# Performance work log

Measured on AMD Instinct MI355X. Metric: run time of the kernel, lower is better.

## Reference

```python
import jax, jax.numpy as jnp
import numpy as np

R = 32            # voxel resolution
DIM = 240         # channels C
EPS_NORM = 0.0    # module eps
BN_EPS = 1e-5     # torch BatchNorm1d default eps


def setup_inputs() -> dict:
    key = jax.random.key(0)
    k1, k2, k3 = jax.random.split(key, 3)
    B, C, N = 4, DIM, 32768
    features = jax.random.normal(k1, (B, C, N), jnp.float32)
    coords = jax.random.uniform(k2, (B, 3, N), jnp.float32)
    # mlp params: Conv1d(2C -> C, kernel 1) + BatchNorm1d(C)
    w = jax.random.normal(k3, (C, 2 * C), jnp.float32) / np.sqrt(2 * C).astype(np.float32)
    b = jnp.zeros((C,), jnp.float32)
    gamma = jnp.ones((C,), jnp.float32)
    beta = jnp.zeros((C,), jnp.float32)
    return {"features": features, "coords": coords, "w": w, "b": b, "gamma": gamma, "beta": beta}


def _voxelize(features, coords):
    # normalize coords into [0, 1], scale to voxel grid
    nc = coords - coords.mean(axis=2, keepdims=True)                      # [B,3,N]
    scale = jnp.linalg.norm(nc, axis=1, keepdims=True).max(axis=2, keepdims=True) * 2.0 + EPS_NORM
    nc = nc / scale + 0.5
    nc = jnp.clip(nc * R, 0, R - 1)
    vox = jnp.round(nc).astype(jnp.int32)
    pos = vox[:, 0] + vox[:, 1] * R + vox[:, 2] * (R * R)                 # [B,N] flattened voxel id
    R3 = R * R * R

    def per_batch(f, p):
        # f: [C,N], p: [N] -> [2C, R3]; per-voxel max feature + second (min) feature
        mx = jax.ops.segment_max(f.T, p, num_segments=R3)                 # [R3, C]
        mn = jax.ops.segment_min(f.T, p, num_segments=R3)                 # [R3, C]
        cnt = jax.ops.segment_sum(jnp.ones_like(p), p, num_segments=R3)  # [R3]
        mask = (cnt > 0)[:, None]
        mx = jnp.where(mask, mx, 0.0)
        mn = jnp.where(mask, mn, 0.0)
        return jnp.concatenate([mx, mn], axis=1).T                        # [2C, R3]

    fea = jax.vmap(per_batch)(features, pos)                              # [B,2C,R3]
    return fea, nc


def reference(features, coords, w, b, gamma, beta):
    fea, nc = _voxelize(features, coords)
    # 1x1 Conv1d (pointwise GEMM) + BatchNorm1d (training-mode batch stats) + Swish
    y = jnp.einsum('co,bov->bcv', w, fea) + b[None, :, None]
    mean = y.mean(axis=(0, 2), keepdims=True)
    var = y.var(axis=(0, 2), keepdims=True)
    y = gamma[None, :, None] * (y - mean) * jax.lax.rsqrt(var + BN_EPS) + beta[None, :, None]
    y = y * jax.nn.sigmoid(y)
    B, C, _ = features.shape
    return y.reshape(B, C, R, R, R), nc
```

## Files before the change

kernel.cpp:

```cpp
#include <hip/hip_runtime.h>
#include <cstdint>
#include <cstddef>

#define RR 32
#define R3 32768
#define NPT 32768
#define CH 240
#define CH2 480
#define NB 4
#define Y_ELEMS 31457280

typedef __attribute__((ext_vector_type(8))) short short8v;
typedef __attribute__((ext_vector_type(4))) float float4v;

union u8pack { short8v v; unsigned short u[8]; };

static __device__ __forceinline__ float bf2f(unsigned short u) {
  return __uint_as_float(((unsigned int)u) << 16);
}
static __device__ __forceinline__ unsigned short f2bf(float f) {
  unsigned int u = __float_as_uint(f);
  u = (u + 0x7FFFu + ((u >> 16) & 1u)) >> 16;
  return (unsigned short)u;
}

static __device__ __forceinline__ void gl_lds16(const void* g, void* l) {
  __builtin_amdgcn_global_load_lds((const __attribute__((address_space(1))) unsigned int*)g,
                                   (__attribute__((address_space(3))) unsigned int*)l, 16, 0, 0);
}

__global__ void k_init(int* __restrict__ cnt, float* __restrict__ stats,
                       const float* __restrict__ w, unsigned short* __restrict__ wfrag) {
  int g = blockIdx.x * 256 + threadIdx.x;
  if (g < NB * R3) cnt[g] = 0;
  if (g < 1024) stats[g] = 0.0f;
  if (g < 14400) {
    int kc = g / 960, rem = g % 960;
    int m = rem >> 6, l = rem & 63;
    int ln = l & 15, q = l >> 4;
    const float* src = w + (size_t)(m * 16 + ln) * CH2 + kc * 32 + q * 8;
    u8pack pk;
#pragma unroll
    for (int j = 0; j < 8; j++) pk.u[j] = f2bf(src[j]);
    *(short8v*)&wfrag[(size_t)g * 8] = pk.v;
  }
}

__global__ __launch_bounds__(1024) void k_coord_stats(const float* __restrict__ coords,
                                                      float* __restrict__ ms) {
  __shared__ float red[1024];
  __shared__ float mean[3];
  int b = blockIdx.x, t = threadIdx.x;
  const float4* cb4 = (const float4*)(coords + (size_t)b * 3 * NPT);
  float s[3] = {0.f, 0.f, 0.f};
  for (int i = t; i < NPT / 4; i += 1024) {
#pragma unroll
    for (int d = 0; d < 3; d++) {
      float4 v = cb4[d * (NPT / 4) + i];
      s[d] += (v.x + v.y) + (v.z + v.w);
    }
  }
  for (int d = 0; d < 3; d++) {
    red[t] = s[d]; __syncthreads();
    for (int k = 512; k > 0; k >>= 1) { if (t < k) red[t] += red[t + k]; __syncthreads(); }
    if (t == 0) mean[d] = red[0] * (1.0f / NPT);
    __syncthreads();
  }
  float m0 = mean[0], m1 = mean[1], m2 = mean[2];
  float mx = 0.f;
  for (int i = t; i < NPT / 4; i += 1024) {
    float4 x = cb4[i], y = cb4[NPT / 4 + i], z = cb4[2 * (NPT / 4) + i];
    float dx, dy, dz, n;
    dx = x.x - m0; dy = y.x - m1; dz = z.x - m2; n = dx * dx + dy * dy + dz * dz; mx = fmaxf(mx, n);
    dx = x.y - m0; dy = y.y - m1; dz = z.y - m2; n = dx * dx + dy * dy + dz * dz; mx = fmaxf(mx, n);
    dx = x.z - m0; dy = y.z - m1; dz = z.z - m2; n = dx * dx + dy * dy + dz * dz; mx = fmaxf(mx, n);
    dx = x.w - m0; dy = y.w - m1; dz = z.w - m2; n = dx * dx + dy * dy + dz * dz; mx = fmaxf(mx, n);
  }
  red[t] = mx; __syncthreads();
  for (int k = 512; k > 0; k >>= 1) { if (t < k) red[t] = fmaxf(red[t], red[t + k]); __syncthreads(); }
  if (t == 0) {
    ms[b * 4 + 0] = m0; ms[b * 4 + 1] = m1; ms[b * 4 + 2] = m2;
    ms[b * 4 + 3] = sqrtf(red[0]) * 2.0f;
  }
}

__global__ void k_pos_nc(const float* __restrict__ coords, const float* __restrict__ ms,
                         float* __restrict__ ncout, int* __restrict__ pos, int* __restrict__ cnt) {
  int g = blockIdx.x * 256 + threadIdx.x;
  int b = g >> 15, i = g & (NPT - 1);
  const float* cb = coords + (size_t)b * 3 * NPT;
  float scale = ms[b * 4 + 3];
  int vox[3];
#pragma unroll
  for (int d = 0; d < 3; d++) {
    float v = (cb[(size_t)d * NPT + i] - ms[b * 4 + d]) / scale + 0.5f;
    v = fminf(fmaxf(v * (float)RR, 0.0f), (float)(RR - 1));
    ncout[((size_t)(b * 3 + d)) * NPT + i] = v;
    vox[d] = (int)rintf(v);
  }
  int p = (b << 15) | (vox[0] + (vox[1] << 5) + (vox[2] << 10));
  pos[g] = p;
  atomicAdd(&cnt[p], 1);
}

__global__ void k_scan(const int* __restrict__ cnt, int* __restrict__ offs) {
  __shared__ int part[1024];
  int b = blockIdx.x, t = threadIdx.x;
  const int base = b * R3;
  int local[32];
  int s = 0;
#pragma unroll
  for (int j = 0; j < 32; j++) { local[j] = cnt[base + t * 32 + j]; s += local[j]; }
  part[t] = s; __syncthreads();
  for (int d = 1; d < 1024; d <<= 1) {
    int v = (t >= d) ? part[t - d] : 0;
    __syncthreads();
    part[t] += v;
    __syncthreads();
  }
  int run = (t == 0) ? 0 : part[t - 1];
#pragma unroll
  for (int j = 0; j < 32; j++) { offs[base + t * 32 + j] = run; run += local[j]; }
}

__global__ void k_scatter(const int* __restrict__ pos, int* __restrict__ offs,
                          int* __restrict__ sorted) {
  int g = blockIdx.x * 256 + threadIdx.x;
  int p = pos[g];
  int slot = atomicAdd(&offs[p], 1);
  sorted[((g >> 15) << 15) + slot] = g;
}

__global__ void k_transpose3(const float* __restrict__ f, unsigned short* __restrict__ ft) {
  __shared__ float tile[CH * 65];
  int p0 = blockIdx.x * 64, b = blockIdx.y;
  int t = threadIdx.x;
  {
    int pp = t & 63, cq = t >> 6;
    const float* src = f + ((size_t)b * CH) * NPT + p0 + pp;
#pragma unroll 4
    for (int j = 0; j < 60; ++j) {
      int c = j * 4 + cq;
      tile[c * 65 + pp] = src[(size_t)c * NPT];
    }
  }
  __syncthreads();
  int ch8 = t & 7;
#pragma unroll
  for (int pass = 0; pass < 2; ++pass) {
    int p = pass * 32 + (t >> 3);
    unsigned short* dst = ft + ((size_t)(b * NPT + p0 + p)) * CH;
#pragma unroll
    for (int i = 0; i < 4; ++i) {
      int ch = ch8 + 8 * i;
      if (ch < 30) {
        u8pack pk;
#pragma unroll
        for (int jj = 0; jj < 8; ++jj) pk.u[jj] = f2bf(tile[(ch * 8 + jj) * 65 + p]);
        *(short8v*)&dst[ch * 8] = pk.v;
      }
    }
  }
}

__global__ __launch_bounds__(256) void k_voxel4(const int* __restrict__ cnt,
                                                const int* __restrict__ offs,
                                                const int* __restrict__ sorted,
                                                const unsigned short* __restrict__ ft,
                                                unsigned short* __restrict__ feaf) {
  __shared__ unsigned short sh[7680];
  int bcg = blockIdx.x;
  int b = bcg >> 11;
  int wave = threadIdx.x >> 6, lane = threadIdx.x & 63;
  int sub = lane >> 5, l = lane & 31;
  int vbase = bcg << 4;
#pragma unroll
  for (int it = 0; it < 2; ++it) {
    int ln = wave + 8 * it + 4 * sub;
    if (l < 30) {
      int v = vbase + ln;
      int t0 = l, t1 = 30 + l;
      int idx0 = (t0 >> 2) * 512 + ((t0 & 3) * 16 + ln) * 8;
      int idx1 = (t1 >> 2) * 512 + ((t1 & 3) * 16 + ln) * 8;
      int n = cnt[v];
      if (n == 0) {
        u8pack z;
#pragma unroll
        for (int j = 0; j < 8; j++) z.u[j] = 0;
        *(short8v*)&sh[idx0] = z.v;
        *(short8v*)&sh[idx1] = z.v;
      } else {
        int start = offs[v] - n;
        const int* sp = sorted + (b << 15) + start;
        float mx[8], mn[8];
#pragma unroll
        for (int j = 0; j < 8; j++) { mx[j] = -__builtin_inff(); mn[j] = __builtin_inff(); }
        int j = 0;
        for (; j + 2 <= n; j += 2) {
          int r0 = sp[j], r1 = sp[j + 1];
          u8pack u0, u1;
          u0.v = *(const short8v*)(ft + (size_t)r0 * CH + l * 8);
          u1.v = *(const short8v*)(ft + (size_t)r1 * CH + l * 8);
#pragma unroll
          for (int k = 0; k < 8; k++) {
            float a = bf2f(u0.u[k]), c = bf2f(u1.u[k]);
            mx[k] = fmaxf(mx[k], fmaxf(a, c));
            mn[k] = fminf(mn[k], fminf(a, c));
          }
        }
        if (j < n) {
          int r0 = sp[j];
          u8pack u0;
          u0.v = *(const short8v*)(ft + (size_t)r0 * CH + l * 8);
#pragma unroll
          for (int k = 0; k < 8; k++) {
            float a = bf2f(u0.u[k]);
            mx[k] = fmaxf(mx[k], a);
            mn[k] = fminf(mn[k], a);
          }
        }
        u8pack omx, omn;
#pragma unroll
        for (int k = 0; k < 8; k++) { omx.u[k] = f2bf(mx[k]); omn.u[k] = f2bf(mn[k]); }
        *(short8v*)&sh[idx0] = omx.v;
        *(short8v*)&sh[idx1] = omn.v;
      }
    }
  }
  __syncthreads();
  unsigned short* dst = feaf + (size_t)bcg * 7680;
  for (int i = threadIdx.x; i < 960; i += 256)
    *(int4*)&dst[i * 8] = *(const int4*)&sh[i * 8];
}

__global__ __launch_bounds__(256, 2) void k_gemm5(const unsigned short* __restrict__ wfrag,
                                                  const unsigned short* __restrict__ feaf,
                                                  const float* __restrict__ bias,
                                                  float* __restrict__ out,
                                                  float* __restrict__ gstats) {
  __shared__ unsigned short wl0[7680];
  __shared__ unsigned short wl1[7680];
  __shared__ float bstats[2 * CH];
  for (int i = threadIdx.x; i < 2 * CH; i += 256) bstats[i] = 0.0f;

  int bz = blockIdx.z;
  int wave = threadIdx.x >> 6, lane = threadIdx.x & 63;
  int ln = lane & 15, q = lane >> 4;
  int v0 = blockIdx.x * 128 + wave * 32;
  int cg0 = v0 >> 4;

  float4v acc[15][2];
#pragma unroll
  for (int m = 0; m < 15; m++) {
    acc[m][0] = (float4v){0.f, 0.f, 0.f, 0.f};
    acc[m][1] = (float4v){0.f, 0.f, 0.f, 0.f};
  }

  const unsigned short* fb = feaf + ((size_t)(bz * 2048 + cg0) * 15) * 512 + lane * 8;

  short8v bc0, bc1, bn0, bn1;
  {
    const unsigned short* gs = wfrag + lane * 8;
    for (int i = wave; i < 15; i += 4) gl_lds16(gs + i * 512, wl0 + i * 512);
    bc0 = *(const short8v*)(fb);
    bc1 = *(const short8v*)(fb + (size_t)15 * 512);
  }

#pragma unroll
  for (int kc = 0; kc < 15; ++kc) {
    __syncthreads();
    if (kc < 14) {
      unsigned short* dstb = ((kc + 1) & 1) ? wl1 : wl0;
      const unsigned short* gs = wfrag + (size_t)(kc + 1) * 7680 + lane * 8;
      for (int i = wave; i < 15; i += 4) gl_lds16(gs + i * 512, dstb + i * 512);
      bn0 = *(const short8v*)(fb + (size_t)(kc + 1) * 512);
      bn1 = *(const short8v*)(fb + (size_t)(15 + kc + 1) * 512);
    }
    const unsigned short* wb = (kc & 1) ? wl1 : wl0;
    const unsigned short* wp = wb + lane * 8;
#pragma unroll
    for (int m = 0; m < 15; ++m) {
      short8v a = *(const short8v*)(wp + m * 512);
      acc[m][0] = __builtin_amdgcn_mfma_f32_16x16x32_bf16(a, bc0, acc[m][0], 0, 0, 0);
      acc[m][1] = __builtin_amdgcn_mfma_f32_16x16x32_bf16(a, bc1, acc[m][1], 0, 0, 0);
    }
    bc0 = bn0; bc1 = bn1;
  }

  float* o0 = out + (size_t)bz * CH * R3 + v0 + ln;
  float* o1 = o0 + 16;
#pragma unroll
  for (int m = 0; m < 15; ++m) {
    int cbase = m * 16 + q * 4;
    float s[4], sq[4];
#pragma unroll
    for (int r = 0; r < 4; ++r) {
      float bb = bias[cbase + r];
      float y0 = acc[m][0][r] + bb;
      float y1 = acc[m][1][r] + bb;
      o0[(size_t)(cbase + r) * R3] = y0;
      o1[(size_t)(cbase + r) * R3] = y1;
      s[r] = y0 + y1;
      sq[r] = y0 * y0 + y1 * y1;
    }
#pragma unroll
    for (int off = 1; off < 16; off <<= 1) {
#pragma unroll
      for (int r = 0; r < 4; ++r) {
        s[r] += __shfl_xor(s[r], off);
        sq[r] += __shfl_xor(sq[r], off);
      }
    }
    if (ln == 0) {
#pragma unroll
      for (int r = 0; r < 4; ++r) {
        atomicAdd(&bstats[cbase + r], s[r]);
        atomicAdd(&bstats[CH + cbase + r], sq[r]);
      }
    }
  }
  __syncthreads();
  for (int i = threadIdx.x; i < 2 * CH; i += 256) atomicAdd(&gstats[i], bstats[i]);
}

__global__ void k_apply(float* __restrict__ y, const float* __restrict__ stats,
                        const float* __restrict__ gamma, const float* __restrict__ beta) {
  int g = blockIdx.x * 256 + threadIdx.x;
  int c = (g >> 13) % CH;
  const float ninv = 1.0f / (float)(NB * R3);
  float mean = stats[c] * ninv;
  float var = stats[CH + c] * ninv - mean * mean;
  float s = gamma[c] * rsqrtf(var + 1e-5f);
  float h = beta[c] - mean * s;
  float4 v = ((const float4*)y)[g];
  float t0 = v.x * s + h; v.x = t0 / (1.0f + __expf(-t0));
  float t1 = v.y * s + h; v.y = t1 / (1.0f + __expf(-t1));
  float t2 = v.z * s + h; v.z = t2 / (1.0f + __expf(-t2));
  float t3 = v.w * s + h; v.w = t3 / (1.0f + __expf(-t3));
  ((float4*)y)[g] = v;
}

extern "C" void kernel_launch(void* const* d_in, const int* in_sizes, int n_in,
                              void* d_out, int out_size, void* d_ws, size_t ws_size,
                              hipStream_t stream) {
  const float* features = (const float*)d_in[0];
  const float* coords   = (const float*)d_in[1];
  const float* w        = (const float*)d_in[2];
  const float* bias     = (const float*)d_in[3];
  const float* gamma    = (const float*)d_in[4];
  const float* beta     = (const float*)d_in[5];
  float* out = (float*)d_out;

  char* ws = (char*)d_ws;
  size_t off = 0;
  float* ms    = (float*)(ws + off); off += 256;
  float* stats = (float*)(ws + off); off += 4096;
  int* pos     = (int*)(ws + off);   off += (size_t)NB * NPT * 4;
  int* cnt     = (int*)(ws + off);   off += (size_t)NB * R3 * 4;
  int* offs    = (int*)(ws + off);   off += (size_t)NB * R3 * 4;
  int* sorted  = (int*)(ws + off);   off += (size_t)NB * NPT * 4;
  unsigned short* wfrag = (unsigned short*)(ws + off); off += (size_t)CH * CH2 * 2;
  unsigned short* ft    = (unsigned short*)(ws + off); off += (size_t)NB * NPT * CH * 2;
  unsigned short* feaf  = (unsigned short*)(ws + off); off += (size_t)NB * R3 * CH2 * 2;

  float* ncout = out + Y_ELEMS;

  k_init<<<516, 256, 0, stream>>>(cnt, stats, w, wfrag);
  k_coord_stats<<<4, 1024, 0, stream>>>(coords, ms);
  k_pos_nc<<<512, 256, 0, stream>>>(coords, ms, ncout, pos, cnt);
  k_scan<<<4, 1024, 0, stream>>>(cnt, offs);
  k_scatter<<<512, 256, 0, stream>>>(pos, offs, sorted);
  k_transpose3<<<dim3(512, 4), 256, 0, stream>>>(features, ft);
  k_voxel4<<<NB * 2048, 256, 0, stream>>>(cnt, offs, sorted, ft, feaf);
  k_gemm5<<<dim3(256, 1, NB), 256, 0, stream>>>(wfrag, feaf, bias, out, stats);
  k_apply<<<Y_ELEMS / 1024, 256, 0, stream>>>(out, stats, gamma, beta);
}
```

Before: 421.7 us.

## Store pre-BN GEMM output as bf16 and retile GEMM with resident weight slice

The GEMM now writes its pre-normalization output as bf16 into a reused workspace buffer instead of fp32 into the final output, and the apply kernel reads bf16 and writes fp32. This halves the intermediate write and read traffic between GEMM and the BN/Swish pass. The GEMM is retiled so each block keeps an 80-channel slice of the weights fully resident in LDS and computes 64 voxels per wave, with the weight fragments reordered to match. That removes the per-k LDS double-buffer syncs, at the cost of reading the features once per channel group and adding bf16 rounding error to the output.

```diff
diff --git a/kernel.cpp b/kernel.cpp
--- a/kernel.cpp
+++ b/kernel.cpp
@@ -35,9 +35,11 @@
   if (g < NB * R3) cnt[g] = 0;
   if (g < 1024) stats[g] = 0.0f;
   if (g < 14400) {
-    int kc = g / 960, rem = g % 960;
-    int m = rem >> 6, l = rem & 63;
-    int ln = l & 15, q = l >> 4;
+    int lane = g & 63, t = g >> 6;
+    int mg = t / 75, r = t % 75;
+    int kc = r / 5, mL = r % 5;
+    int m = mg * 5 + mL;
+    int ln = lane & 15, q = lane >> 4;
     const float* src = w + (size_t)(m * 16 + ln) * CH2 + kc * 32 + q * 8;
     u8pack pk;
 #pragma unroll
@@ -233,111 +235,120 @@
     *(int4*)&dst[i * 8] = *(const int4*)&sh[i * 8];
 }
 
-__global__ __launch_bounds__(256, 2) void k_gemm5(const unsigned short* __restrict__ wfrag,
+__global__ __launch_bounds__(256, 2) void k_gemm6(const unsigned short* __restrict__ wfrag,
                                                   const unsigned short* __restrict__ feaf,
                                                   const float* __restrict__ bias,
-                                                  float* __restrict__ out,
+                                                  unsigned short* __restrict__ ybf,
                                                   float* __restrict__ gstats) {
-  __shared__ unsigned short wl0[7680];
-  __shared__ unsigned short wl1[7680];
-  __shared__ float bstats[2 * CH];
-  for (int i = threadIdx.x; i < 2 * CH; i += 256) bstats[i] = 0.0f;
-
-  int bz = blockIdx.z;
+  __shared__ unsigned short wl[75 * 512];
+  __shared__ float bstats[160];
   int wave = threadIdx.x >> 6, lane = threadIdx.x & 63;
   int ln = lane & 15, q = lane >> 4;
-  int v0 = blockIdx.x * 128 + wave * 32;
+  int mg = blockIdx.y, bz = blockIdx.z;
+
+  for (int i = threadIdx.x; i < 160; i += 256) bstats[i] = 0.0f;
+
+  {
+    const unsigned short* gs = wfrag + (size_t)mg * 75 * 512 + lane * 8;
+    for (int i = wave; i < 75; i += 4) gl_lds16(gs + i * 512, wl + i * 512);
+  }
+
+  int v0 = blockIdx.x * 256 + wave * 64;
   int cg0 = v0 >> 4;
-
-  float4v acc[15][2];
-#pragma unroll
-  for (int m = 0; m < 15; m++) {
-    acc[m][0] = (float4v){0.f, 0.f, 0.f, 0.f};
-    acc[m][1] = (float4v){0.f, 0.f, 0.f, 0.f};
-  }
-
-  const unsigned short* fb = feaf + ((size_t)(bz * 2048 + cg0) * 15) * 512 + lane * 8;
-
-  short8v bc0, bc1, bn0, bn1;
-  {
-    const unsigned short* gs = wfrag + lane * 8;
-    for (int i = wave; i < 15; i += 4) gl_lds16(gs + i * 512, wl0 + i * 512);
-    bc0 = *(const short8v*)(fb);
-    bc1 = *(const short8v*)(fb + (size_t)15 * 512);
-  }
+  const unsigned short* fbb = feaf + ((size_t)(bz * 2048 + cg0) * 15) * 512 + lane * 8;
+
+  float4v acc[5][4];
+#pragma unroll
+  for (int m = 0; m < 5; m++)
+#pragma unroll
+    for (int j = 0; j < 4; j++) acc[m][j] = (float4v){0.f, 0.f, 0.f, 0.f};
+
+  short8v cb0 = *(const short8v*)(fbb + (size_t)(0 * 15 + 0) * 512);
+  short8v cb1 = *(const short8v*)(fbb + (size_t)(1 * 15 + 0) * 512);
+  short8v cb2 = *(const short8v*)(fbb + (size_t)(2 * 15 + 0) * 512);
+  short8v cb3 = *(const short8v*)(fbb + (size_t)(3 * 15 + 0) * 512);
+
+  __syncthreads();
 
 #pragma unroll
   for (int kc = 0; kc < 15; ++kc) {
-    __syncthreads();
+    short8v nb0, nb1, nb2, nb3;
     if (kc < 14) {
-      unsigned short* dstb = ((kc + 1) & 1) ? wl1 : wl0;
-      const unsigned short* gs = wfrag + (size_t)(kc + 1) * 7680 + lane * 8;
-      for (int i = wave; i < 15; i += 4) gl_lds16(gs + i * 512, dstb + i * 512);
-      bn0 = *(const short8v*)(fb + (size_t)(kc + 1) * 512);
-      bn1 = *(const short8v*)(fb + (size_t)(15 + kc + 1) * 512);
-    }
-    const unsigned short* wb = (kc & 1) ? wl1 : wl0;
-    const unsigned short* wp = wb + lane * 8;
-#pragma unroll
-    for (int m = 0; m < 15; ++m) {
-      short8v a = *(const short8v*)(wp + m * 512);
-      acc[m][0] = __builtin_amdgcn_mfma_f32_16x16x32_bf16(a, bc0, acc[m][0], 0, 0, 0);
-      acc[m][1] = __builtin_amdgcn_mfma_f32_16x16x32_bf16(a, bc1, acc[m][1], 0, 0, 0);
-    }
-    bc0 = bn0; bc1 = bn1;
-  }
-
-  float* o0 = out + (size_t)bz * CH * R3 + v0 + ln;
-  float* o1 = o0 + 16;
-#pragma unroll
-  for (int m = 0; m < 15; ++m) {
-    int cbase = m * 16 + q * 4;
-    float s[4], sq[4];
+      nb0 = *(const short8v*)(fbb + (size_t)(0 * 15 + kc + 1) * 512);
+      nb1 = *(const short8v*)(fbb + (size_t)(1 * 15 + kc + 1) * 512);
+      nb2 = *(const short8v*)(fbb + (size_t)(2 * 15 + kc + 1) * 512);
+      nb3 = *(const short8v*)(fbb + (size_t)(3 * 15 + kc + 1) * 512);
+    }
+    const unsigned short* wp = wl + (size_t)(kc * 5) * 512 + lane * 8;
+#pragma unroll
+    for (int mL = 0; mL < 5; ++mL) {
+      short8v a = *(const short8v*)(wp + (size_t)mL * 512);
+      acc[mL][0] = __builtin_amdgcn_mfma_f32_16x16x32_bf16(a, cb0, acc[mL][0], 0, 0, 0);
+      acc[mL][1] = __builtin_amdgcn_mfma_f32_16x16x32_bf16(a, cb1, acc[mL][1], 0, 0, 0);
+      acc[mL][2] = __builtin_amdgcn_mfma_f32_16x16x32_bf16(a, cb2, acc[mL][2], 0, 0, 0);
+      acc[mL][3] = __builtin_amdgcn_mfma_f32_16x16x32_bf16(a, cb3, acc[mL][3], 0, 0, 0);
+    }
+    if (kc < 14) { cb0 = nb0; cb1 = nb1; cb2 = nb2; cb3 = nb3; }
+  }
+
+  unsigned short* yb = ybf + ((size_t)bz * CH) * R3 + v0 + ln;
+#pragma unroll
+  for (int mL = 0; mL < 5; ++mL) {
 #pragma unroll
     for (int r = 0; r < 4; ++r) {
-      float bb = bias[cbase + r];
-      float y0 = acc[m][0][r] + bb;
-      float y1 = acc[m][1][r] + bb;
-      o0[(size_t)(cbase + r) * R3] = y0;
-      o1[(size_t)(cbase + r) * R3] = y1;
-      s[r] = y0 + y1;
-      sq[r] = y0 * y0 + y1 * y1;
-    }
-#pragma unroll
-    for (int off = 1; off < 16; off <<= 1) {
-#pragma unroll
-      for (int r = 0; r < 4; ++r) {
-        s[r] += __shfl_xor(s[r], off);
-        sq[r] += __shfl_xor(sq[r], off);
+      int cl = mL * 16 + q * 4 + r;
+      int c = mg * 80 + cl;
+      float bb = bias[c];
+      float y0 = acc[mL][0][r] + bb;
+      float y1 = acc[mL][1][r] + bb;
+      float y2 = acc[mL][2][r] + bb;
+      float y3 = acc[mL][3][r] + bb;
+      unsigned short* yrow = yb + (size_t)c * R3;
+      yrow[0] = f2bf(y0); yrow[16] = f2bf(y1); yrow[32] = f2bf(y2); yrow[48] = f2bf(y3);
+      float s = (y0 + y1) + (y2 + y3);
+      float sq = (y0 * y0 + y1 * y1) + (y2 * y2 + y3 * y3);
+#pragma unroll
+      for (int off = 1; off < 16; off <<= 1) {
+        s += __shfl_xor(s, off);
+        sq += __shfl_xor(sq, off);
       }
-    }
-    if (ln == 0) {
-#pragma unroll
-      for (int r = 0; r < 4; ++r) {
-        atomicAdd(&bstats[cbase + r], s[r]);
-        atomicAdd(&bstats[CH + cbase + r], sq[r]);
+      if (ln == 0) {
+        atomicAdd(&bstats[cl], s);
+        atomicAdd(&bstats[80 + cl], sq);
       }
     }
   }
   __syncthreads();
-  for (int i = threadIdx.x; i < 2 * CH; i += 256) atomicAdd(&gstats[i], bstats[i]);
-}
-
-__global__ void k_apply(float* __restrict__ y, const float* __restrict__ stats,
-                        const float* __restrict__ gamma, const float* __restrict__ beta) {
+  for (int i = threadIdx.x; i < 160; i += 256) {
+    int g = (i < 80) ? (mg * 80 + i) : (CH + mg * 80 + (i - 80));
+    atomicAdd(&gstats[g], bstats[i]);
+  }
+}
+
+__global__ void k_apply(const unsigned short* __restrict__ ybf, float* __restrict__ out,
+                        const float* __restrict__ stats, const float* __restrict__ gamma,
+                        const float* __restrict__ beta) {
   int g = blockIdx.x * 256 + threadIdx.x;
-  int c = (g >> 13) % CH;
+  int c = (g >> 12) % CH;
   const float ninv = 1.0f / (float)(NB * R3);
   float mean = stats[c] * ninv;
   float var = stats[CH + c] * ninv - mean * mean;
   float s = gamma[c] * rsqrtf(var + 1e-5f);
   float h = beta[c] - mean * s;
-  float4 v = ((const float4*)y)[g];
-  float t0 = v.x * s + h; v.x = t0 / (1.0f + __expf(-t0));
-  float t1 = v.y * s + h; v.y = t1 / (1.0f + __expf(-t1));
-  float t2 = v.z * s + h; v.z = t2 / (1.0f + __expf(-t2));
-  float t3 = v.w * s + h; v.w = t3 / (1.0f + __expf(-t3));
-  ((float4*)y)[g] = v;
+  u8pack v;
+  v.v = *(const short8v*)(ybf + (size_t)g * 8);
+  float4 o0, o1;
+  float t;
+  t = bf2f(v.u[0]) * s + h; o0.x = t / (1.0f + __expf(-t));
+  t = bf2f(v.u[1]) * s + h; o0.y = t / (1.0f + __expf(-t));
+  t = bf2f(v.u[2]) * s + h; o0.z = t / (1.0f + __expf(-t));
+  t = bf2f(v.u[3]) * s + h; o0.w = t / (1.0f + __expf(-t));
+  t = bf2f(v.u[4]) * s + h; o1.x = t / (1.0f + __expf(-t));
+  t = bf2f(v.u[5]) * s + h; o1.y = t / (1.0f + __expf(-t));
+  t = bf2f(v.u[6]) * s + h; o1.z = t / (1.0f + __expf(-t));
+  t = bf2f(v.u[7]) * s + h; o1.w = t / (1.0f + __expf(-t));
+  ((float4*)out)[(size_t)g * 2] = o0;
+  ((float4*)out)[(size_t)g * 2 + 1] = o1;
 }
 
 extern "C" void kernel_launch(void* const* d_in, const int* in_sizes, int n_in,
@@ -362,6 +373,7 @@
   unsigned short* wfrag = (unsigned short*)(ws + off); off += (size_t)CH * CH2 * 2;
   unsigned short* ft    = (unsigned short*)(ws + off); off += (size_t)NB * NPT * CH * 2;
   unsigned short* feaf  = (unsigned short*)(ws + off); off += (size_t)NB * R3 * CH2 * 2;
+  unsigned short* ybf   = ft;
 
   float* ncout = out + Y_ELEMS;
 
@@ -372,6 +384,6 @@
   k_scatter<<<512, 256, 0, stream>>>(pos, offs, sorted);
   k_transpose3<<<dim3(512, 4), 256, 0, stream>>>(features, ft);
   k_voxel4<<<NB * 2048, 256, 0, stream>>>(cnt, offs, sorted, ft, feaf);
-  k_gemm5<<<dim3(256, 1, NB), 256, 0, stream>>>(wfrag, feaf, bias, out, stats);
-  k_apply<<<Y_ELEMS / 1024, 256, 0, stream>>>(out, stats, gamma, beta);
-}
+  k_gemm6<<<dim3(128, 3, NB), 256, 0, stream>>>(wfrag, feaf, bias, ybf, stats);
+  k_apply<<<Y_ELEMS / 2048, 256, 0, stream>>>(ybf, out, stats, gamma, beta);
+}
```

Result: faster. 399.8 us (-5.2%).
